# Performance work log

Hardware: AMD Instinct MI355X
Metric: run time of the kernel (lower is better)

Reference implementation:

```python
import jax, jax.numpy as jnp
import numpy as np

G = 64        # grid_size
S = 4         # num_samples along perpendicular axis
C = 771       # feature_channels
NH = 3        # n_heads
NV = 4        # number of camera views
HF = WF = 64  # image feature map size
B = 1
QD = 3 * C    # query_dim of TriplaneAttention


def bilin(img, gx, gy, padding):
    """Bilinear grid_sample, align_corners=True. img [C,H,W]; gx,gy normalized [-1,1]."""
    Ci, H, W = img.shape
    ix = (gx + 1.0) * 0.5 * (W - 1)
    iy = (gy + 1.0) * 0.5 * (H - 1)
    if padding == 'border':
        ix = jnp.clip(ix, 0, W - 1)
        iy = jnp.clip(iy, 0, H - 1)
    x0 = jnp.floor(ix); y0 = jnp.floor(iy)
    x1 = x0 + 1.0;      y1 = y0 + 1.0
    wx = ix - x0;       wy = iy - y0
    img2 = img.reshape(Ci, H * W)
    def gather(xi, yi):
        xc = jnp.clip(xi, 0, W - 1).astype(jnp.int32)
        yc = jnp.clip(yi, 0, H - 1).astype(jnp.int32)
        vals = jnp.take(img2, (yc * W + xc).reshape(-1), axis=1).reshape((Ci,) + xi.shape)
        if padding == 'zeros':
            valid = ((xi >= 0) & (xi <= W - 1) & (yi >= 0) & (yi <= H - 1)).astype(img.dtype)
            vals = vals * valid
        return vals
    return (gather(x0, y0) * ((1 - wx) * (1 - wy)) + gather(x1, y0) * (wx * (1 - wy))
            + gather(x0, y1) * ((1 - wx) * wy) + gather(x1, y1) * (wx * wy))


def sample_points_along_axis(plane):
    x = jnp.linspace(-1.0, 1.0, G)
    gx, gy = jnp.meshgrid(x, x, indexing='xy')  # [G,G]
    samp = jnp.linspace(-1.0, 1.0, S)
    ex = jnp.broadcast_to(gx[..., None], (G, G, S))
    ey = jnp.broadcast_to(gy[..., None], (G, G, S))
    es = jnp.broadcast_to(samp[None, None, :], (G, G, S))
    if plane == 'xy':
        return jnp.stack([ex, ey, es], axis=-1)
    elif plane == 'xz':
        return jnp.stack([ex, es, ey], axis=-1)
    else:
        return jnp.stack([es, ex, ey], axis=-1)


def project_to_other_planes(points, plane, queries):
    # points [G,G,S,3]; queries = [q_xy, q_xz, q_yz] each [G,G,C]
    idx = {'xy': 0, 'xz': 1, 'yz': 2}
    sel = {'xy': (0, 1), 'xz': (0, 2), 'yz': (1, 2)}
    feats = []
    for other in ['xy', 'xz', 'yz']:
        if other == plane:
            continue
        a, b = sel[other]
        coords = jnp.stack([points[..., a], points[..., b]], axis=-1)
        # Faithful to original: pixel-range coords passed as normalized grid, border padding
        g = jnp.clip((coords * 0.5 + 0.5) * (G - 1), 0, G - 1)
        pf = queries[idx[other]].transpose(2, 0, 1)  # [C,G,G]
        s = bilin(pf, g[..., 0], g[..., 1], 'border')  # [C,G,G,S]
        feats.append(s.transpose(1, 2, 3, 0))          # [G,G,S,C]
    return jnp.concatenate(feats, axis=2)              # [G,G,2S,C]


def layernorm(x, g, b):
    mu = jnp.mean(x, axis=-1, keepdims=True)
    var = jnp.mean((x - mu) ** 2, axis=-1, keepdims=True)
    return (x - mu) / jnp.sqrt(var + 1e-5) * g + b


def triplane_attention(query, context, Wk, bk, Wv, bv, ln_g, ln_b):
    # query [B,N,QD]; context [B,N,L,C]
    Bq, N, L, _ = context.shape
    DH = QD // NH
    q = layernorm(query, ln_g, ln_b).reshape(Bq, N, NH, DH)
    k = (context @ Wk + bk).reshape(Bq, N, L, NH, DH)
    v = (context @ Wv + bv).reshape(Bq, N, L, NH, DH)
    scores = jnp.einsum('bnlhd,bnhd->bhnl', k, q)   # no 1/sqrt(d) scaling (faithful)
    w = jax.nn.softmax(scores, axis=-1)
    out = jnp.einsum('bhnl,bnlhd->bnhd', w, v)
    return out.reshape(Bq, N, QD)


def setup_inputs():
    key = jax.random.key(0)
    ks = jax.random.split(key, 12)
    image_features = jax.random.normal(ks[0], (B, NV, C, HF, WF), jnp.float32)
    depths = jax.random.uniform(ks[1], (B, NV, HF, WF), jnp.float32)
    # cameras: identity rotation, w2c translation [dx,0,3] -> c2w translation [-dx,0,-3]
    offs = np.linspace(-0.2, 0.2, NV).astype(np.float32)
    c2w = np.tile(np.eye(4, dtype=np.float32), (B, NV, 1, 1))
    for m in range(NV):
        c2w[:, m, 0, 3] = -offs[m]
        c2w[:, m, 2, 3] = -3.0
    K = np.zeros((B, NV, 3, 3), np.float32)
    K[:, :, 0, 0] = WF; K[:, :, 1, 1] = HF
    K[:, :, 0, 2] = WF / 2; K[:, :, 1, 2] = HF / 2; K[:, :, 2, 2] = 1.0
    pointclouds = jax.random.uniform(ks[2], (B, 4096, 3), jnp.float32, minval=-1.0, maxval=1.0)
    q_xy = jax.random.normal(ks[3], (G, G, C), jnp.float32) * 0.02
    q_xz = jax.random.normal(ks[4], (G, G, C), jnp.float32) * 0.02
    q_yz = jax.random.normal(ks[5], (G, G, C), jnp.float32) * 0.02
    Wk = jax.random.normal(ks[6], (C, QD), jnp.float32) * 0.02
    bk = jnp.zeros((QD,), jnp.float32)
    Wv = jax.random.normal(ks[7], (C, QD), jnp.float32) * 0.02
    bv = jnp.zeros((QD,), jnp.float32)
    ln_g = jnp.ones((QD,), jnp.float32)
    ln_b = jnp.zeros((QD,), jnp.float32)
    return dict(image_features=image_features, depths=depths, c2w_cond=jnp.asarray(c2w),
                intrinsic_cond=jnp.asarray(K), pointclouds=pointclouds,
                q_xy=q_xy, q_xz=q_xz, q_yz=q_yz, Wk=Wk, bk=bk, Wv=Wv, bv=bv,
                ln_g=ln_g, ln_b=ln_b)


def _forward(image_features, c2w_cond, intrinsic_cond, q_xy, q_xz, q_yz,
             Wk, bk, Wv, bv, ln_g, ln_b):
    queries = [q_xy, q_xz, q_yz]
    w2c = jnp.linalg.inv(c2w_cond)  # [B,NV,4,4]

    def project(pts, w2c_b, K_b):
        # pts [N,3]; returns u,v,mask each [N,NV]
        ph = jnp.concatenate([pts, jnp.ones_like(pts[:, :1])], axis=-1)
        cam = jnp.einsum('nl,mkl->nmk', ph, w2c_b)      # [N,NV,4]
        depth = cam[..., 2]
        uvh = jnp.einsum('nmk,mhk->nmh', cam[..., :3], K_b)
        ds = depth + 1e-8
        u = uvh[..., 0] / ds
        v = uvh[..., 1] / ds
        mask = (depth > 0) & (u >= 0) & (u < WF) & (v >= 0) & (v < HF)
        return u, v, mask

    def sample_views(feats_b, u_b, v_b, mask_b):
        # feats_b [NV,C,HF,WF]; u_b,v_b [N,NV] -> [N,NV,C]
        gx = 2.0 * (u_b / (WF - 1)) - 1.0
        gy = 2.0 * (v_b / (HF - 1)) - 1.0
        samp = jax.vmap(lambda img, x, y: bilin(img, x, y, 'zeros'))(feats_b, gx.T, gy.T)  # [NV,C,N]
        samp = samp.transpose(2, 0, 1)  # [N,NV,C]
        return samp * mask_b[..., None].astype(samp.dtype)

    outs = []
    for pi, plane in enumerate(['xy', 'xz', 'yz']):
        points = sample_points_along_axis(plane)           # [G,G,S,3]
        pts = points.reshape(-1, 3)                        # [G*G*S,3]
        u, v, mask = jax.vmap(lambda w, k: project(pts, w, k))(w2c, intrinsic_cond)  # [B,N,NV]
        samp = jax.vmap(sample_views)(image_features, u, v, mask)  # [B,N,NV,C]
        ctx = samp.reshape(B, G * G, S * NV, C)
        other = project_to_other_planes(points, plane, queries)    # [G,G,2S,C]
        q = jnp.concatenate([queries[pi],
                             jnp.mean(other[:, :, :S], axis=2),
                             jnp.mean(other[:, :, S:], axis=2)], axis=-1).reshape(G * G, QD)
        q = jnp.broadcast_to(q[None], (B, G * G, QD))
        out = triplane_attention(q, ctx, Wk, bk, Wv, bv, ln_g, ln_b)
        outs.append(out.reshape(B, G, G, QD))
    return tuple(outs)


def reference(image_features, depths, c2w_cond, intrinsic_cond, pointclouds,
              q_xy, q_xz, q_yz, Wk, bk, Wv, bv, ln_g, ln_b):
    return _forward(image_features, c2w_cond, intrinsic_cond,
                    q_xy, q_xz, q_yz, Wk, bk, Wv, bv, ln_g, ln_b)
```

## Files before the change

kernel.cpp:

```cpp
#include <hip/hip_runtime.h>
#include <math.h>


constexpr int kG = 64, kS = 4, kC = 771, kNV = 4;
constexpr int kQD = 2313;
constexpr int kNPIX = 4096;
constexpr int kL = 16;
constexpr int kImgMStride = kC * kG * kG;
constexpr int kKP = 800;
constexpr int kLDA = 2400;
constexpr int kBROWS = 896;
constexpr int kCP = 776;
constexpr int kNG = kCP / 4;
constexpr int kLDQ = 3 * kCP;
constexpr int kIMS2 = kNPIX * kCP;

constexpr size_t kQKB_FLOATS = (size_t)kNPIX * kLDQ;
constexpr size_t kW_ELEMS = (size_t)3 * kBROWS * kKP;
constexpr size_t kA0_ELEMS = (size_t)kNPIX * kKP;
constexpr size_t kWH_ELEMS = (size_t)kNPIX * kLDA;
constexpr size_t kQN_FLOATS = (size_t)kNPIX * kQD;
constexpr size_t kTAB_FLOATS = (size_t)6 * 64 * kC;

using bf16x8 = __attribute__((ext_vector_type(8))) short;
using f32x4 = __attribute__((ext_vector_type(4))) float;

__device__ __forceinline__ unsigned short f2bf(float x) {
  unsigned int u = __float_as_uint(x);
  u = (u + 0x7FFFu + ((u >> 16) & 1u)) >> 16;
  return (unsigned short)u;
}
__device__ __forceinline__ float bf2f(unsigned short h) {
  return __uint_as_float(((unsigned int)h) << 16);
}
__device__ __forceinline__ void gload16(const unsigned short* g,
                                        unsigned short* l) {
  __builtin_amdgcn_global_load_lds(
      (const __attribute__((address_space(1))) void*)g,
      (__attribute__((address_space(3))) void*)l, 16, 0, 0);
}

__global__ void invert4_kernel(const float* __restrict__ c2w,
                               float* __restrict__ w2c) {
  const int m = threadIdx.x;
  if (m >= kNV) return;
  float a[4][8];
  for (int r = 0; r < 4; ++r)
    for (int c = 0; c < 4; ++c) {
      a[r][c] = c2w[m * 16 + r * 4 + c];
      a[r][4 + c] = (r == c) ? 1.f : 0.f;
    }
  for (int col = 0; col < 4; ++col) {
    int piv = col;
    float best = fabsf(a[col][col]);
    for (int r = col + 1; r < 4; ++r) {
      float t = fabsf(a[r][col]);
      if (t > best) { best = t; piv = r; }
    }
    if (piv != col)
      for (int c = 0; c < 8; ++c) {
        float t = a[col][c]; a[col][c] = a[piv][c]; a[piv][c] = t;
      }
    const float inv = 1.f / a[col][col];
    for (int c = 0; c < 8; ++c) a[col][c] *= inv;
    for (int r = 0; r < 4; ++r)
      if (r != col) {
        const float f = a[r][col];
        for (int c = 0; c < 8; ++c) a[r][c] -= f * a[col][c];
      }
  }
  for (int r = 0; r < 4; ++r)
    for (int c = 0; c < 4; ++c) w2c[m * 16 + r * 4 + c] = a[r][4 + c];
}

__global__ void __launch_bounds__(256) transpose_img_kernel(
    const float* __restrict__ img, float* __restrict__ out) {
  __shared__ float t[64][65];
  const int y = blockIdx.x, m = blockIdx.y, tid = threadIdx.x;
  const size_t obase = ((size_t)m * kNPIX + (size_t)y * 64) * kCP;
  for (int c0 = 0; c0 < kC; c0 += 64) {
    const int cw = (kC - c0) < 64 ? (kC - c0) : 64;
    for (int idx = tid; idx < cw * 64; idx += 256) {
      const int cl = idx >> 6, x = idx & 63;
      t[cl][x] = img[(((size_t)m * kC + c0 + cl) * 64 + y) * 64 + x];
    }
    __syncthreads();
    for (int idx = tid; idx < 64 * 64; idx += 256) {
      const int x = idx >> 6, cl = idx & 63;
      if (cl < cw) out[obase + (size_t)x * kCP + c0 + cl] = t[cl][x];
    }
    __syncthreads();
  }
  for (int idx = tid; idx < 64 * 8; idx += 256) {
    const int x = idx >> 3, c = 768 + (idx & 7);
    if (c >= kC && c < kCP) out[obase + (size_t)x * kCP + c] = 0.f;
  }
}

__global__ void __launch_bounds__(256) prep_wk_kernel(
    const float* __restrict__ Wk, unsigned short* __restrict__ hi,
// ... 23 lines not shown
    const int j = j0 + ty, k = k0 + tx;
    if (j < kBROWS && k < kKP) {
      const float v = t[tx][ty];
      const unsigned short a = f2bf(v);
      const size_t p = ((size_t)h * kBROWS + j) * kKP + k;
      hi[p] = a;
      lo[p] = f2bf(v - bf2f(a));
    }
  }
}

__global__ void __launch_bounds__(256) prep_meantab_kernel(
    const float* __restrict__ q_xy, const float* __restrict__ q_xz,
    const float* __restrict__ q_yz, float* __restrict__ tab) {
  const int v = blockIdx.x;
  const int t = blockIdx.y;
  const int plane = t >> 1, part = t & 1;
  const float* src;
  if (plane == 0) src = part ? q_yz : q_xz;
  else if (plane == 1) src = part ? q_yz : q_xy;
  else src = part ? q_xz : q_xy;
  __shared__ int sIdx[4][4];
  __shared__ float sW[4][4];
  if (threadIdx.x < 4) {
    const int s = threadIdx.x;
    const float Xv = -1.f + 2.f * v / 63.f;
    const float Ts = -1.f + 2.f * s / 3.f;
    float a, b;
    if (plane == 0) { a = Xv; b = Ts; }
    else if (plane == 1) {
      if (part == 0) { a = Xv; b = Ts; } else { a = Ts; b = Xv; }
    } else { a = Ts; b = Xv; }
    const float ga = fminf(fmaxf((a * 0.5f + 0.5f) * 63.f, 0.f), 63.f);
    const float gb = fminf(fmaxf((b * 0.5f + 0.5f) * 63.f, 0.f), 63.f);
    const float ix = fminf(fmaxf((ga + 1.f) * 0.5f * 63.f, 0.f), 63.f);
    const float iy = fminf(fmaxf((gb + 1.f) * 0.5f * 63.f, 0.f), 63.f);
    const float x0 = floorf(ix), y0 = floorf(iy);
    const float wx = ix - x0, wy = iy - y0;
    const int x0i = (int)x0, y0i = (int)y0;
    const int x1i = (x0i + 1 > 63) ? 63 : x0i + 1;
    const int y1i = (y0i + 1 > 63) ? 63 : y0i + 1;
    sIdx[s][0] = (y0i * 64 + x0i) * kC;
    sIdx[s][1] = (y0i * 64 + x1i) * kC;
    sIdx[s][2] = (y1i * 64 + x0i) * kC;
    sIdx[s][3] = (y1i * 64 + x1i) * kC;
    sW[s][0] = (1.f - wx) * (1.f - wy);
    sW[s][1] = wx * (1.f - wy);
    sW[s][2] = (1.f - wx) * wy;
    sW[s][3] = wx * wy;
  }
  __syncthreads();
  for (int c = threadIdx.x; c < kC; c += 256) {
    float a1 = 0.f;
#pragma unroll
    for (int s = 0; s < 4; ++s) {
      a1 += src[sIdx[s][0] + c] * sW[s][0] + src[sIdx[s][1] + c] * sW[s][1]
          + src[sIdx[s][2] + c] * sW[s][2] + src[sIdx[s][3] + c] * sW[s][3];
    }
    tab[((size_t)t * 64 + v) * kC + c] = a1 * 0.25f;
  }
}

__global__ void __launch_bounds__(256) prep_tabsplit_kernel(
    const float* __restrict__ tab, const float* __restrict__ ln_g,
    unsigned short* __restrict__ hi, unsigned short* __restrict__ lo) {
  const int v = blockIdx.x;
  const int t = blockIdx.y;
  const int h = 1 + (t & 1);
  const size_t base = ((size_t)t * 128 + v) * kKP;
  for (int k = threadIdx.x; k < kKP; k += 256) {
    float val = 0.f;
    if (v < 64 && k < kC)
      val = tab[((size_t)t * 64 + v) * kC + k] * ln_g[h * kC + k];
    const unsigned short a = f2bf(val);
    hi[base + k] = a;
    lo[base + k] = f2bf(val - bf2f(a));
  }
}

__global__ void __launch_bounds__(256) prep_uv_kernel(
    const float* __restrict__ Wk, const float* __restrict__ ln_g,
    const float* __restrict__ ln_b, float* __restrict__ u,
    float* __restrict__ v) {
  const int c = blockIdx.x * 256 + threadIdx.x;
  const int h = blockIdx.y;
  if (c >= kCP) return;
  float su = 0.f, sv = 0.f;
  if (c < kC) {
    const float* wr = Wk + (size_t)c * kQD + h * kC;
    const float* g = ln_g + h * kC;
    const float* b = ln_b + h * kC;
    for (int k = 0; k < kC; ++k) {
      su = fmaf(wr[k], g[k], su);
      sv = fmaf(wr[k], b[k], sv);
    }
  }
  u[h * kCP + c] = su;
  v[h * kCP + c] = sv;
}

__global__ void __launch_bounds__(256) build_a0_kernel(
    const float* __restrict__ q_xy, const float* __restrict__ q_xz,
    const float* __restrict__ q_yz, const float* __restrict__ tab,
    const float* __restrict__ ln_g, const float* __restrict__ ln_b,
    const float* __restrict__ bk, unsigned short* __restrict__ a0hi,
    unsigned short* __restrict__ a0lo, float* __restrict__ murs,
    float* __restrict__ qbk) {
  const int slot = blockIdx.y, plane = slot;
  const float* qp = (plane == 0) ? q_xy : (plane == 1) ? q_xz : q_yz;
  const int n = blockIdx.x, i = n >> 6, j = n & 63, tid = threadIdx.x;
  __shared__ float qf[kQD];
  __shared__ float red[16];

  const float* t0 = tab + ((size_t)(plane * 2 + 0) * 64 + j) * kC;
  const float* t1 = tab + ((size_t)(plane * 2 + 1) * 64 + i) * kC;
  for (int c = tid; c < kC; c += 256) {
    qf[c] = qp[(size_t)n * kC + c];
    qf[kC + c] = t0[c];
    qf[2 * kC + c] = t1[c];
  }
  __syncthreads();

  float sm = 0.f;
  for (int idx = tid; idx < kQD; idx += 256) sm += qf[idx];
#pragma unroll
  for (int off = 32; off; off >>= 1) sm += __shfl_down(sm, off);
  if ((tid & 63) == 0) red[tid >> 6] = sm;
  __syncthreads();
  const float mu = (red[0] + red[1] + red[2] + red[3]) * (1.f / kQD);
  __syncthreads();
  float sq = 0.f;
  for (int idx = tid; idx < kQD; idx += 256) {
    const float d = qf[idx] - mu;
    sq += d * d;
  }
#pragma unroll
  for (int off = 32; off; off >>= 1) sq += __shfl_down(sq, off);
  if ((tid & 63) == 0) red[tid >> 6] = sq;
  __syncthreads();
  const float var = (red[0] + red[1] + red[2] + red[3]) * (1.f / kQD);
  const float rstd = 1.f / sqrtf(var + 1e-5f);
  if (tid == 0) {
    murs[2 * ((size_t)slot * kNPIX + n)] = mu;
    murs[2 * ((size_t)slot * kNPIX + n) + 1] = rstd;
  }
  __syncthreads();

  float h0 = 0.f, h1 = 0.f, h2 = 0.f;
  unsigned short* ah = a0hi + (size_t)slot * kA0_ELEMS + (size_t)n * kKP;
  unsigned short* al = a0lo + (size_t)slot * kA0_ELEMS + (size_t)n * kKP;
  for (int idx = tid; idx < 3 * kKP; idx += 256) {
    int h, k;
    if (idx < kKP) { h = 0; k = idx; }
    else if (idx < 2 * kKP) { h = 1; k = idx - kKP; }
    else { h = 2; k = idx - 2 * kKP; }
    if (k < kC) {
      const int li = h * kC + k;
      const float v = (qf[li] - mu) * rstd * ln_g[li] + ln_b[li];
      const float pb = v * bk[li];
      if (h == 0) h0 += pb; else if (h == 1) h1 += pb; else h2 += pb;
    }
    if (idx < kKP) {
      const float y = (idx < kC) ? qf[idx] * ln_g[idx] : 0.f;
      const unsigned short hv = f2bf(y);
      ah[idx] = hv;
      al[idx] = f2bf(y - bf2f(hv));
    }
  }
#pragma unroll
  for (int off = 32; off; off >>= 1) {
    h0 += __shfl_down(h0, off);
    h1 += __shfl_down(h1, off);
    h2 += __shfl_down(h2, off);
  }
  if ((tid & 63) == 0) {
    red[(tid >> 6) * 4 + 0] = h0;
    red[(tid >> 6) * 4 + 1] = h1;
    red[(tid >> 6) * 4 + 2] = h2;
  }
  __syncthreads();
  if (tid < 3)
    qbk[((size_t)slot * kNPIX + n) * 3 + tid] =
        red[tid] + red[4 + tid] + red[8 + tid] + red[12 + tid];
}

__global__ void __launch_bounds__(256) gemm_a0_kernel(
    const unsigned short* __restrict__ A0hi,
    const unsigned short* __restrict__ A0lo,
    const unsigned short* __restrict__ Bhi,
    const unsigned short* __restrict__ Blo, const float* __restrict__ murs,
    const float* __restrict__ uvec, const float* __restrict__ vvec,
    float* __restrict__ qkb) {
  __shared__ unsigned short smA[2][128 * 32];
  __shared__ unsigned short smB[2][128 * 32];
  const int slot = blockIdx.z;
  const int t = blockIdx.y * 7 + blockIdx.x;
  const int xcd = t & 7, idx = t >> 3;
  const int nb = idx % 7, mb = (xcd << 2) + idx / 7;
  const int m0 = mb * 128, n0 = nb * 128;
  const unsigned short* Ah = A0hi + (size_t)slot * kA0_ELEMS;
  const unsigned short* Al = A0lo + (size_t)slot * kA0_ELEMS;
  const int tid = threadIdx.x;
  const int lane = tid & 63, w = tid >> 6;
  const int wm = w >> 1, wn = w & 1;

  const int sr0 = w * 16 + (lane >> 2);
  const int ss = lane & 3;
  size_t aoff[2], boff[2];
  int ldsb[2];
#pragma unroll
  for (int p = 0; p < 2; ++p) {
    const int r = p * 64 + sr0;
    const int kl = (ss ^ ((r >> 1) & 3)) * 8;
    aoff[p] = (size_t)(m0 + r) * kKP + kl;
    boff[p] = (size_t)(n0 + r) * kKP + kl;
    ldsb[p] = (p * 64 + w * 16) * 32;
  }
  int offA[4], offB[4];
#pragma unroll
  for (int i = 0; i < 4; ++i) {
    const int ra = wm * 64 + i * 16 + (lane & 15);
    offA[i] = ra * 32 + (((lane >> 4) ^ ((ra >> 1) & 3)) << 3);
    const int rb = wn * 64 + i * 16 + (lane & 15);
    offB[i] = rb * 32 + (((lane >> 4) ^ ((rb >> 1) & 3)) << 3);
  }
  f32x4 acc[4][4];
#pragma unroll
  for (int i = 0; i < 4; ++i)
#pragma unroll
    for (int j = 0; j < 4; ++j) acc[i][j] = f32x4{0.f, 0.f, 0.f, 0.f};

  for (int k0 = 0; k0 < kKP; k0 += 32) {
#pragma unroll
    for (int p = 0; p < 2; ++p) {
      gload16(Ah + aoff[p] + k0, &smA[0][ldsb[p]]);
      gload16(Al + aoff[p] + k0, &smA[1][ldsb[p]]);
      gload16(Bhi + boff[p] + k0, &smB[0][ldsb[p]]);
      gload16(Blo + boff[p] + k0, &smB[1][ldsb[p]]);
    }
    __syncthreads();
    bf16x8 ah[4], al[4], bh[4], bl[4];
#pragma unroll
    for (int i = 0; i < 4; ++i) {
      ah[i] = *(const bf16x8*)&smA[0][offA[i]];
      al[i] = *(const bf16x8*)&smA[1][offA[i]];
      bh[i] = *(const bf16x8*)&smB[0][offB[i]];
      bl[i] = *(const bf16x8*)&smB[1][offB[i]];
    }
#pragma unroll
    for (int i = 0; i < 4; ++i)
#pragma unroll
      for (int j = 0; j < 4; ++j)
        acc[i][j] = __builtin_amdgcn_mfma_f32_16x16x32_bf16(ah[i], bh[j],
                                                            acc[i][j], 0, 0, 0);
#pragma unroll
    for (int i = 0; i < 4; ++i)
#pragma unroll
      for (int j = 0; j < 4; ++j)
        acc[i][j] = __builtin_amdgcn_mfma_f32_16x16x32_bf16(ah[i], bl[j],
                                                            acc[i][j], 0, 0, 0);
#pragma unroll
    for (int i = 0; i < 4; ++i)
#pragma unroll
      for (int j = 0; j < 4; ++j)
        acc[i][j] = __builtin_amdgcn_mfma_f32_16x16x32_bf16(al[i], bh[j],
                                                            acc[i][j], 0, 0, 0);
    __syncthreads();
  }

  const float* mr = murs + 2 * ((size_t)slot * kNPIX);
  float* dst = qkb + (size_t)slot * kQKB_FLOATS;
  const int rbase = m0 + wm * 64;
  const int cbase = n0 + wn * 64;
#pragma unroll
  for (int i = 0; i < 4; ++i) {
#pragma unroll
    for (int j = 0; j < 4; ++j) {
      const int col = cbase + j * 16 + (lane & 15);
      if (col < kC) {
        const float uu = uvec[col], vv = vvec[col];
#pragma unroll
        for (int r = 0; r < 4; ++r) {
          const int row = rbase + i * 16 + (lane >> 4) * 4 + r;
          const float mu = mr[2 * row], rs = mr[2 * row + 1];
          dst[(size_t)row * kLDQ + col] =
              rs * acc[i][j][r] - rs * mu * uu + vv;
        }
      } else if (col < kCP) {
#pragma unroll
        for (int r = 0; r < 4; ++r) {
          const int row = rbase + i * 16 + (lane >> 4) * 4 + r;
          dst[(size_t)row * kLDQ + col] = 0.f;
        }
      }
    }
  }
}

__global__ void __launch_bounds__(256) gemm_tab_kernel(
    const unsigned short* __restrict__ Thi,
    const unsigned short* __restrict__ Tlo,
    const unsigned short* __restrict__ Wkhi,
    const unsigned short* __restrict__ Wklo, float* __restrict__ Atab) {
  __shared__ unsigned short smA[2][128 * 32];
  __shared__ unsigned short smB[2][128 * 32];
  const int t = blockIdx.y;
  const int n0 = blockIdx.x * 128;
  const int h = 1 + (t & 1);
  const unsigned short* Ah = Thi + (size_t)t * 128 * kKP;
  const unsigned short* Al = Tlo + (size_t)t * 128 * kKP;
  const unsigned short* Bh = Wkhi + (size_t)h * kBROWS * kKP;
  const unsigned short* Bl = Wklo + (size_t)h * kBROWS * kKP;
  const int tid = threadIdx.x;
  const int lane = tid & 63, w = tid >> 6;
  const int wm = w >> 1, wn = w & 1;

  const int sr0 = w * 16 + (lane >> 2);
  const int ss = lane & 3;
  size_t aoff[2], boff[2];
  int ldsb[2];
#pragma unroll
  for (int p = 0; p < 2; ++p) {
    const int r = p * 64 + sr0;
    const int kl = (ss ^ ((r >> 1) & 3)) * 8;
    aoff[p] = (size_t)r * kKP + kl;
    boff[p] = (size_t)(n0 + r) * kKP + kl;
    ldsb[p] = (p * 64 + w * 16) * 32;
  }
  int offA[4], offB[4];
#pragma unroll
  for (int i = 0; i < 4; ++i) {
    const int ra = wm * 64 + i * 16 + (lane & 15);
    offA[i] = ra * 32 + (((lane >> 4) ^ ((ra >> 1) & 3)) << 3);
    const int rb = wn * 64 + i * 16 + (lane & 15);
    offB[i] = rb * 32 + (((lane >> 4) ^ ((rb >> 1) & 3)) << 3);
  }
  f32x4 acc[4][4];
#pragma unroll
  for (int i = 0; i < 4; ++i)
#pragma unroll
    for (int j = 0; j < 4; ++j) acc[i][j] = f32x4{0.f, 0.f, 0.f, 0.f};

  for (int k0 = 0; k0 < kKP; k0 += 32) {
#pragma unroll
    for (int p = 0; p < 2; ++p) {
      gload16(Ah + aoff[p] + k0, &smA[0][ldsb[p]]);
      gload16(Al + aoff[p] + k0, &smA[1][ldsb[p]]);
      gload16(Bh + boff[p] + k0, &smB[0][ldsb[p]]);
      gload16(Bl + boff[p] + k0, &smB[1][ldsb[p]]);
    }
    __syncthreads();
    bf16x8 ah[4], al[4], bh[4], bl[4];
#pragma unroll
    for (int i = 0; i < 4; ++i) {
      ah[i] = *(const bf16x8*)&smA[0][offA[i]];
      al[i] = *(const bf16x8*)&smA[1][offA[i]];
      bh[i] = *(const bf16x8*)&smB[0][offB[i]];
      bl[i] = *(const bf16x8*)&smB[1][offB[i]];
    }
#pragma unroll
    for (int i = 0; i < 4; ++i)
#pragma unroll
      for (int j = 0; j < 4; ++j)
        acc[i][j] = __builtin_amdgcn_mfma_f32_16x16x32_bf16(ah[i], bh[j],
                                                            acc[i][j], 0, 0, 0);
#pragma unroll
    for (int i = 0; i < 4; ++i)
#pragma unroll
      for (int j = 0; j < 4; ++j)
        acc[i][j] = __builtin_amdgcn_mfma_f32_16x16x32_bf16(ah[i], bl[j],
                                                            acc[i][j], 0, 0, 0);
#pragma unroll
    for (int i = 0; i < 4; ++i)
#pragma unroll
      for (int j = 0; j < 4; ++j)
        acc[i][j] = __builtin_amdgcn_mfma_f32_16x16x32_bf16(al[i], bh[j],
                                                            acc[i][j], 0, 0, 0);
    __syncthreads();
  }

  float* C = Atab + (size_t)t * 128 * kCP;
  const int rbase = wm * 64;
  const int cbase = n0 + wn * 64;
#pragma unroll
  for (int i = 0; i < 4; ++i) {
#pragma unroll
    for (int j = 0; j < 4; ++j) {
      const int col = cbase + j * 16 + (lane & 15);
      if (col < kCP) {
        const float keep = (col < kC) ? 1.f : 0.f;
#pragma unroll
        for (int r = 0; r < 4; ++r) {
          const int row = rbase + i * 16 + (lane >> 4) * 4 + r;
          C[(size_t)row * kCP + col] = acc[i][j][r] * keep;
        }
      }
    }
  }
}

__global__ void __launch_bounds__(256) combine_qk_kernel(
    const float* __restrict__ Atab, const float* __restrict__ u,
    const float* __restrict__ v, const float* __restrict__ murs,
    float* __restrict__ qkb) {
  const int slot = blockIdx.y, n = blockIdx.x;
  const int i = n >> 6, j = n & 63, tid = threadIdx.x;
  const float mu = murs[2 * ((size_t)slot * kNPIX + n)];
  const float rs = murs[2 * ((size_t)slot * kNPIX + n) + 1];
  const float rsmu = rs * mu;
  float* dst = qkb + (size_t)slot * kQKB_FLOATS + (size_t)n * kLDQ;
  const float* A1 = Atab + ((size_t)(slot * 2 + 0) * 128 + j) * kCP;
  const float* A2 = Atab + ((size_t)(slot * 2 + 1) * 128 + i) * kCP;
  if (tid < kNG) {
    const int c4 = tid << 2;
    const float4 a1 = *(const float4*)&A1[c4];
    const float4 u1 = *(const float4*)&u[kCP + c4];
    const float4 v1 = *(const float4*)&v[kCP + c4];
    float4 r1;
    r1.x = rs * a1.x - rsmu * u1.x + v1.x;
    r1.y = rs * a1.y - rsmu * u1.y + v1.y;
    r1.z = rs * a1.z - rsmu * u1.z + v1.z;
    r1.w = rs * a1.w - rsmu * u1.w + v1.w;
    *(float4*)&dst[kCP + c4] = r1;
    const float4 a2 = *(const float4*)&A2[c4];
    const float4 u2 = *(const float4*)&u[2 * kCP + c4];
    const float4 v2 = *(const float4*)&v[2 * kCP + c4];
    float4 r2;
    r2.x = rs * a2.x - rsmu * u2.x + v2.x;
    r2.y = rs * a2.y - rsmu * u2.y + v2.y;
    r2.z = rs * a2.z - rsmu * u2.z + v2.z;
    r2.w = rs * a2.w - rsmu * u2.w + v2.w;
    *(float4*)&dst[2 * kCP + c4] = r2;
  }
}

__global__ void __launch_bounds__(512, 6) sample_attn4_kernel(
    const float* __restrict__ imgt, const float* __restrict__ w2c,
    const float* __restrict__ Kin, const float* __restrict__ qkb,
    const float* __restrict__ qbk, const int plane_base,
    unsigned short* __restrict__ whi) {
  __shared__ __align__(16) float ctx[kL][kCP];
  __shared__ float sW2[kL][4];
  __shared__ int sI2[kL][4];
  __shared__ float sscp[2][48];
  __shared__ float ssc[48], swt[48];
  const int slot = blockIdx.y, plane = plane_base + slot;
  const int bid = blockIdx.x;
  const int n = ((bid & 7) << 9) | (bid >> 3);
  const int i = n >> 6, j = n & 63, tid = threadIdx.x;
  const float* qkn = qkb + (size_t)slot * kQKB_FLOATS + (size_t)n * kLDQ;

  if (tid < kL) {
    const int s = tid >> 2, m = tid & 3;
    const float Xi = -1.f + 2.f * i / 63.f;
    const float Xj = -1.f + 2.f * j / 63.f;
    const float Ts = -1.f + 2.f * s / 3.f;
    float px, py, pz;
    if (plane == 0) { px = Xj; py = Xi; pz = Ts; }
    else if (plane == 1) { px = Xj; py = Ts; pz = Xi; }
    else { px = Ts; py = Xj; pz = Xi; }
    const float* W = w2c + m * 16;
    const float c0 = W[0] * px + W[1] * py + W[2] * pz + W[3];
    const float c1 = W[4] * px + W[5] * py + W[6] * pz + W[7];
    const float c2 = W[8] * px + W[9] * py + W[10] * pz + W[11];
    const float* Km = Kin + m * 9;
    const float un = Km[0] * c0 + Km[1] * c1 + Km[2] * c2;
    const float vn = Km[3] * c0 + Km[4] * c1 + Km[5] * c2;
    const float ds = c2 + 1e-8f;
    const float u = un / ds, v = vn / ds;
    const bool mk =
        (c2 > 0.f && u >= 0.f && u < 64.f && v >= 0.f && v < 64.f);
    float w00 = 0.f, w10 = 0.f, w01 = 0.f, w11 = 0.f;
    int i00 = 0, i10 = 0, i01 = 0, i11 = 0;
    if (mk) {
      const float gx = 2.f * (u / 63.f) - 1.f;
      const float gy = 2.f * (v / 63.f) - 1.f;
      const float ix = (gx + 1.f) * 0.5f * 63.f;
      const float iy = (gy + 1.f) * 0.5f * 63.f;
      const float x0 = floorf(ix), y0 = floorf(iy);
      const float x1 = x0 + 1.f, y1 = y0 + 1.f;
      const float wx = ix - x0, wy = iy - y0;
      const float v00 = (x0 >= 0.f && x0 <= 63.f && y0 >= 0.f && y0 <= 63.f) ? 1.f : 0.f;
      const float v10 = (x1 >= 0.f && x1 <= 63.f && y0 >= 0.f && y0 <= 63.f) ? 1.f : 0.f;
      const float v01 = (x0 >= 0.f && x0 <= 63.f && y1 >= 0.f && y1 <= 63.f) ? 1.f : 0.f;
      const float v11 = (x1 >= 0.f && x1 <= 63.f && y1 >= 0.f && y1 <= 63.f) ? 1.f : 0.f;
      w00 = (1.f - wx) * (1.f - wy) * v00;
      w10 = wx * (1.f - wy) * v10;
      w01 = (1.f - wx) * wy * v01;
      w11 = wx * wy * v11;
      const int x0i = (int)fminf(fmaxf(x0, 0.f), 63.f);
      const int x1i = (int)fminf(fmaxf(x1, 0.f), 63.f);
      const int y0i = (int)fminf(fmaxf(y0, 0.f), 63.f);
      const int y1i = (int)fminf(fmaxf(y1, 0.f), 63.f);
      const int mb = m * kIMS2;
      i00 = mb + (y0i * 64 + x0i) * kCP;
      i10 = mb + (y0i * 64 + x1i) * kCP;
      i01 = mb + (y1i * 64 + x0i) * kCP;
      i11 = mb + (y1i * 64 + x1i) * kCP;
    }
    sI2[tid][0] = i00; sI2[tid][1] = i10; sI2[tid][2] = i01; sI2[tid][3] = i11;
    sW2[tid][0] = w00; sW2[tid][1] = w10; sW2[tid][2] = w01; sW2[tid][3] = w11;
  }
  __syncthreads();

  const int lane = tid & 63, wv = tid >> 6;
#pragma unroll
  for (int q = 0; q < 2; ++q) {
    const int l = (wv << 1) + q;
    const float a0 = sW2[l][0], a1 = sW2[l][1], a2 = sW2[l][2], a3 = sW2[l][3];
    const int b0 = sI2[l][0], b1 = sI2[l][1], b2 = sI2[l][2], b3 = sI2[l][3];
    for (int g = lane; g < kNG; g += 64) {
      const int c4 = g << 2;
      const float4 t0 = *(const float4*)&imgt[b0 + c4];
      const float4 t1 = *(const float4*)&imgt[b1 + c4];
      const float4 t2 = *(const float4*)&imgt[b2 + c4];
      const float4 t3 = *(const float4*)&imgt[b3 + c4];
      float4 r;
      r.x = fmaf(t0.x, a0, fmaf(t1.x, a1, fmaf(t2.x, a2, t3.x * a3)));
      r.y = fmaf(t0.y, a0, fmaf(t1.y, a1, fmaf(t2.y, a2, t3.y * a3)));
      r.z = fmaf(t0.z, a0, fmaf(t1.z, a1, fmaf(t2.z, a2, t3.z * a3)));
      r.w = fmaf(t0.w, a0, fmaf(t1.w, a1, fmaf(t2.w, a2, t3.w * a3)));
      *(float4*)&ctx[l][c4] = r;
    }
  }
  __syncthreads();

  const int g16 = tid >> 4, l16 = tid & 15;
  const float* qbkn = qbk + ((size_t)slot * kNPIX + n) * 3;
  {
    const int l = g16 & 15, half = g16 >> 4;
    float p0 = 0.f, p1 = 0.f, p2 = 0.f;
#pragma unroll
    for (int it = 0; it < 6; ++it) {
      const int c4 = (l16 + ((2 * it + half) << 4)) << 2;
      const float4 cv = *(const float4*)&ctx[l][c4];
      const float4 q0 = *(const float4*)&qkn[c4];
      const float4 q1 = *(const float4*)&qkn[kCP + c4];
      const float4 q2 = *(const float4*)&qkn[2 * kCP + c4];
      p0 = fmaf(cv.x, q0.x, fmaf(cv.y, q0.y, fmaf(cv.z, q0.z, fmaf(cv.w, q0.w, p0))));
      p1 = fmaf(cv.x, q1.x, fmaf(cv.y, q1.y, fmaf(cv.z, q1.z, fmaf(cv.w, q1.w, p1))));
      p2 = fmaf(cv.x, q2.x, fmaf(cv.y, q2.y, fmaf(cv.z, q2.z, fmaf(cv.w, q2.w, p2))));
    }
    if (half == 0 && l16 < 2) {
      const int c4 = (192 + l16) << 2;
      const float4 cv = *(const float4*)&ctx[l][c4];
      const float4 q0 = *(const float4*)&qkn[c4];
      const float4 q1 = *(const float4*)&qkn[kCP + c4];
      const float4 q2 = *(const float4*)&qkn[2 * kCP + c4];
      p0 = fmaf(cv.x, q0.x, fmaf(cv.y, q0.y, fmaf(cv.z, q0.z, fmaf(cv.w, q0.w, p0))));
      p1 = fmaf(cv.x, q1.x, fmaf(cv.y, q1.y, fmaf(cv.z, q1.z, fmaf(cv.w, q1.w, p1))));
      p2 = fmaf(cv.x, q2.x, fmaf(cv.y, q2.y, fmaf(cv.z, q2.z, fmaf(cv.w, q2.w, p2))));
    }
#pragma unroll
    for (int off = 8; off; off >>= 1) {
      p0 += __shfl_down(p0, off, 16);
      p1 += __shfl_down(p1, off, 16);
      p2 += __shfl_down(p2, off, 16);
    }
    if (l16 == 0) {
      sscp[half][l] = p0;
      sscp[half][16 + l] = p1;
      sscp[half][32 + l] = p2;
    }
  }
  __syncthreads();
  if (tid < 48) ssc[tid] = sscp[0][tid] + sscp[1][tid] + qbkn[tid >> 4];
  __syncthreads();
  if (tid < 3) {
    float mx = ssc[tid * 16];
#pragma unroll
    for (int l = 1; l < kL; ++l) mx = fmaxf(mx, ssc[tid * 16 + l]);
    float e[kL];
    float sum = 0.f;
#pragma unroll
    for (int l = 0; l < kL; ++l) {
      e[l] = expf(ssc[tid * 16 + l] - mx);
      sum += e[l];
    }
    const float inv = 1.f / sum;
#pragma unroll
    for (int l = 0; l < kL; ++l) swt[tid * 16 + l] = e[l] * inv;
  }
  __syncthreads();

  unsigned short* wh = whi + (size_t)slot * kWH_ELEMS + (size_t)n * kLDA;
  if (tid < 2 * kNG) {
    const int c4 = (tid >> 1) << 2;
    const int l0 = (tid & 1) << 3;
    float4 o0{0.f, 0.f, 0.f, 0.f}, o1{0.f, 0.f, 0.f, 0.f},
        o2{0.f, 0.f, 0.f, 0.f};
#pragma unroll
    for (int dl = 0; dl < 8; ++dl) {
      const int l = l0 + dl;
      const float4 cv = *(const float4*)&ctx[l][c4];
      const float s0 = swt[l], s1 = swt[16 + l], s2 = swt[32 + l];
      o0.x = fmaf(cv.x, s0, o0.x); o0.y = fmaf(cv.y, s0, o0.y);
      o0.z = fmaf(cv.z, s0, o0.z); o0.w = fmaf(cv.w, s0, o0.w);
      o1.x = fmaf(cv.x, s1, o1.x); o1.y = fmaf(cv.y, s1, o1.y);
      o1.z = fmaf(cv.z, s1, o1.z); o1.w = fmaf(cv.w, s1, o1.w);
      o2.x = fmaf(cv.x, s2, o2.x); o2.y = fmaf(cv.y, s2, o2.y);
      o2.z = fmaf(cv.z, s2, o2.z); o2.w = fmaf(cv.w, s2, o2.w);
    }
    o0.x += __shfl_xor(o0.x, 1); o0.y += __shfl_xor(o0.y, 1);
    o0.z += __shfl_xor(o0.z, 1); o0.w += __shfl_xor(o0.w, 1);
    o1.x += __shfl_xor(o1.x, 1); o1.y += __shfl_xor(o1.y, 1);
    o1.z += __shfl_xor(o1.z, 1); o1.w += __shfl_xor(o1.w, 1);
    o2.x += __shfl_xor(o2.x, 1); o2.y += __shfl_xor(o2.y, 1);
    o2.z += __shfl_xor(o2.z, 1); o2.w += __shfl_xor(o2.w, 1);
    if ((tid & 1) == 0) {
      float4 ov[3] = {o0, o1, o2};
#pragma unroll
      for (int h = 0; h < 3; ++h) {
        ushort4 hi;
        hi.x = f2bf(ov[h].x);
        hi.y = f2bf(ov[h].y);
        hi.z = f2bf(ov[h].z);
        hi.w = f2bf(ov[h].w);
        *(ushort4*)&wh[h * kKP + c4] = hi;
      }
    }
  }
  if (tid < 72) {
    const int h = tid / 24, k2 = kCP + tid % 24;
    wh[h * kKP + k2] = 0;
  }
}

__global__ void __launch_bounds__(256) gemm_out_kernel(
    const unsigned short* __restrict__ Ahi,
    const unsigned short* __restrict__ Bhi,
    const unsigned short* __restrict__ Blo, float* __restrict__ C,
    const float* __restrict__ bias) {
  __shared__ unsigned short smA[128 * 32];
  __shared__ unsigned short smB[2][128 * 32];
  const int slot = blockIdx.z / 3, h = blockIdx.z % 3;
  const int t = blockIdx.y * 7 + blockIdx.x;
  const int xcd = t & 7, idx = t >> 3;
  const int nb = idx % 7, mb = (xcd << 2) + idx / 7;
  const int m0 = mb * 128, n0 = nb * 128;
  const unsigned short* Ah = Ahi + (size_t)slot * kWH_ELEMS;
  float* Cs = C + (size_t)slot * kQN_FLOATS;
  const int tid = threadIdx.x;
  const int lane = tid & 63, w = tid >> 6;
  const int wm = w >> 1, wn = w & 1;

// ... 341 lines not shown
      float v = 0.f;
      if (k0 + kk < K) v = A[(size_t)(m0 + mm) * lda + hoff + k0 + kk];
      As[kk][mm] = v;
    }
    if (BT) {
#pragma unroll
      for (int p = 0; p < 4; ++p) {
        const int idx = tid + p * 256;
        const int jj = idx >> 4, kk = idx & 15;
        float v = 0.f;
        if ((n0 + jj) < N && (k0 + kk) < K)
          v = B[(size_t)(n0 + jj) * ldb + hoff + k0 + kk];
        Bs[kk][jj] = v;
      }
    } else {
#pragma unroll
      for (int p = 0; p < 4; ++p) {
        const int idx = tid + p * 256;
        const int kk = idx >> 6, jj = idx & 63;
        float v = 0.f;
        if ((n0 + jj) < N && (k0 + kk) < K)
          v = B[(size_t)(k0 + kk) * ldb + hoff + n0 + jj];
        Bs[kk][jj] = v;
      }
    }
    __syncthreads();
#pragma unroll
    for (int kk = 0; kk < BK; ++kk) {
      float a[8], b[4];
#pragma unroll
      for (int r = 0; r < 8; ++r) a[r] = As[kk][ty * 8 + r];
#pragma unroll
      for (int c = 0; c < 4; ++c) b[c] = Bs[kk][tx * 4 + c];
#pragma unroll
      for (int r = 0; r < 8; ++r)
#pragma unroll
        for (int c = 0; c < 4; ++c) acc[r][c] = fmaf(a[r], b[c], acc[r][c]);
    }
    __syncthreads();
  }
#pragma unroll
  for (int r = 0; r < 8; ++r) {
    const int mm = m0 + ty * 8 + r;
    if (mm >= M) continue;
#pragma unroll
    for (int c = 0; c < 4; ++c) {
      const int jj = n0 + tx * 4 + c;
      if (jj < N) {
        float v = acc[r][c];
        if (BIAS) v += bias[hoff + jj];
        Cp[(size_t)mm * ldc + hoff + jj] = v;
      }
    }
  }
}

extern "C" void kernel_launch(void* const* d_in, const int* in_sizes, int n_in,
                              void* d_out, int out_size, void* d_ws,
                              size_t ws_size, hipStream_t stream) {
  const float* imgf = (const float*)d_in[0];
  const float* c2w = (const float*)d_in[2];
  const float* Kin = (const float*)d_in[3];
  const float* qpl[3] = {(const float*)d_in[5], (const float*)d_in[6],
                         (const float*)d_in[7]};
  const float* Wk = (const float*)d_in[8];
  const float* bk = (const float*)d_in[9];
  const float* Wv = (const float*)d_in[10];
  const float* bv = (const float*)d_in[11];
  const float* ln_g = (const float*)d_in[12];
  const float* ln_b = (const float*)d_in[13];
  float* out = (float*)d_out;
  char* wsb = (char*)d_ws;

  const size_t IMGT_FLOATS = (size_t)kNV * kIMS2;

  size_t off = 0;
  auto take = [&](size_t bytes) {
    size_t p = off;
    off = (off + bytes + 511) & ~(size_t)511;
    return p;
  };
  const size_t o_w2c = take(64 * 4);
  const size_t o_qbk = take((size_t)3 * kNPIX * 3 * 4);
  const size_t o_qkb = take((size_t)3 * kQKB_FLOATS * 4);
  const size_t o_wkhi = take(kW_ELEMS * 2);
  const size_t o_wklo = take(kW_ELEMS * 2);
  const size_t o_wvthi = take(kW_ELEMS * 2);
  const size_t o_wvtlo = take(kW_ELEMS * 2);
  const size_t o_a0hi = take((size_t)3 * kA0_ELEMS * 2);
  const size_t o_a0lo = take((size_t)3 * kA0_ELEMS * 2);
  const size_t o_whi = take((size_t)3 * kWH_ELEMS * 2);
  const size_t o_murs = take((size_t)3 * kNPIX * 2 * 4);
  const size_t o_u = take((size_t)3 * kCP * 4);
  const size_t o_v = take((size_t)3 * kCP * 4);
  const size_t o_tab = take(kTAB_FLOATS * 4);
  const size_t o_tshi = take((size_t)6 * 128 * kKP * 2);
  const size_t o_tslo = take((size_t)6 * 128 * kKP * 2);
  const size_t o_atab = take((size_t)6 * 128 * kCP * 4);
  const size_t o_imgt = take(IMGT_FLOATS * 4);
  const size_t need = off;

  if (ws_size >= need) {
    float* w2c = (float*)(wsb + o_w2c);
    float* qbk = (float*)(wsb + o_qbk);
    float* qkb = (float*)(wsb + o_qkb);
    unsigned short* wkhi = (unsigned short*)(wsb + o_wkhi);
    unsigned short* wklo = (unsigned short*)(wsb + o_wklo);
    unsigned short* wvthi = (unsigned short*)(wsb + o_wvthi);
    unsigned short* wvtlo = (unsigned short*)(wsb + o_wvtlo);
    unsigned short* a0hi = (unsigned short*)(wsb + o_a0hi);
    unsigned short* a0lo = (unsigned short*)(wsb + o_a0lo);
    unsigned short* whi = (unsigned short*)(wsb + o_whi);
    float* murs = (float*)(wsb + o_murs);
    float* uvec = (float*)(wsb + o_u);
    float* vvec = (float*)(wsb + o_v);
    float* meantab = (float*)(wsb + o_tab);
    unsigned short* tshi = (unsigned short*)(wsb + o_tshi);
    unsigned short* tslo = (unsigned short*)(wsb + o_tslo);
    float* atab = (float*)(wsb + o_atab);
    float* imgt = (float*)(wsb + o_imgt);

    invert4_kernel<<<1, 64, 0, stream>>>(c2w, w2c);
    prep_wk_kernel<<<dim3(kBROWS, 3), 256, 0, stream>>>(Wk, wkhi, wklo);
    prep_wvt_kernel<<<dim3(13, 14, 3), 256, 0, stream>>>(Wv, wvthi, wvtlo);
    prep_meantab_kernel<<<dim3(64, 6), 256, 0, stream>>>(qpl[0], qpl[1],
                                                         qpl[2], meantab);
    prep_tabsplit_kernel<<<dim3(128, 6), 256, 0, stream>>>(meantab, ln_g,
                                                           tshi, tslo);
    prep_uv_kernel<<<dim3(4, 3), 256, 0, stream>>>(Wk, ln_g, ln_b, uvec,
                                                   vvec);
    transpose_img_kernel<<<dim3(64, kNV), 256, 0, stream>>>(imgf, imgt);
    gemm_tab_kernel<<<dim3(7, 6), 256, 0, stream>>>(tshi, tslo, wkhi, wklo,
                                                    atab);
    build_a0_kernel<<<dim3(kNPIX, 3), 256, 0, stream>>>(
        qpl[0], qpl[1], qpl[2], meantab, ln_g, ln_b, bk, a0hi, a0lo, murs,
        qbk);
    gemm_a0_kernel<<<dim3(7, 32, 3), 256, 0, stream>>>(
        a0hi, a0lo, wkhi, wklo, murs, uvec, vvec, qkb);
    combine_qk_kernel<<<dim3(kNPIX, 3), 256, 0, stream>>>(atab, uvec, vvec,
                                                          murs, qkb);
    sample_attn4_kernel<<<dim3(kNPIX, 3), 512, 0, stream>>>(
        imgt, w2c, Kin, qkb, qbk, 0, whi);
    gemm_out_kernel<<<dim3(7, 32, 9), 256, 0, stream>>>(whi, wvthi, wvtlo,
                                                        out, bv);
  } else {
    float* ws = (float*)d_ws;
    const size_t OFF_QBK = 64;
    const size_t OFF_BIG = OFF_QBK + (size_t)kNPIX * 3;
    float* w2c = ws;
    float* qbk = ws + OFF_QBK;
    float* qn = ws + OFF_BIG;
    float* qkb = qn + kQN_FLOATS;

    invert4_kernel<<<1, 64, 0, stream>>>(c2w, w2c);
    for (int p = 0; p < 3; ++p) {
      build_q_f32<<<kNPIX, 256, 0, stream>>>(qpl[0], qpl[1], qpl[2], p, ln_g,
                                             ln_b, bk, qn, qbk);
      gemm_f32<true, false><<<dim3(13, 32, 3), 256, 0, stream>>>(
          qn, Wk, qkb, nullptr, kNPIX, kC, kC, kQD, kQD, kQD, kC);
      sample_attn_f32<<<kNPIX, 256, 0, stream>>>(imgf, w2c, Kin, qkb, qbk, p,
                                                 qn);
      gemm_f32<false, true><<<dim3(13, 32, 3), 256, 0, stream>>>(
          qn, Wv, out + (size_t)p * kQN_FLOATS, bv, kNPIX, kC, kC, kQD, kQD,
          kQD, kC);
    }
  }
}
```

Measured before the change: 710.9 us.

## Fuse q/k combine into attention kernel and parallelize u/v prep reduction

Removes the combine_qk kernel that wrote full per-pixel q·Wk for the two mean-derived heads. The attention kernel now reads the small shared table rows, u and v directly and applies the per-pixel scale algebraically after the dot products. This cuts a large intermediate buffer write and read in exchange for more dot products per context row. It also rewrites prep_uv so each block reduces one output column across threads instead of having one thread loop serially over all 771 inputs.

```diff
diff --git a/kernel.cpp b/kernel.cpp
--- a/kernel.cpp
+++ b/kernel.cpp
@@ -12,10 +12,9 @@
 constexpr int kBROWS = 896;
 constexpr int kCP = 776;
 constexpr int kNG = kCP / 4;
-constexpr int kLDQ = 3 * kCP;
 constexpr int kIMS2 = kNPIX * kCP;
 
-constexpr size_t kQKB_FLOATS = (size_t)kNPIX * kLDQ;
+constexpr size_t kQ0_FLOATS = (size_t)kNPIX * kCP;
 constexpr size_t kW_ELEMS = (size_t)3 * kBROWS * kKP;
 constexpr size_t kA0_ELEMS = (size_t)kNPIX * kKP;
 constexpr size_t kWH_ELEMS = (size_t)kNPIX * kLDA;
@@ -205,21 +204,34 @@
     const float* __restrict__ Wk, const float* __restrict__ ln_g,
     const float* __restrict__ ln_b, float* __restrict__ u,
     float* __restrict__ v) {
-  const int c = blockIdx.x * 256 + threadIdx.x;
+  const int c = blockIdx.x;
   const int h = blockIdx.y;
-  if (c >= kCP) return;
+  __shared__ float ru[4], rv[4];
   float su = 0.f, sv = 0.f;
   if (c < kC) {
     const float* wr = Wk + (size_t)c * kQD + h * kC;
     const float* g = ln_g + h * kC;
     const float* b = ln_b + h * kC;
-    for (int k = 0; k < kC; ++k) {
-      su = fmaf(wr[k], g[k], su);
-      sv = fmaf(wr[k], b[k], sv);
-    }
-  }
-  u[h * kCP + c] = su;
-  v[h * kCP + c] = sv;
+    for (int k = threadIdx.x; k < kC; k += 256) {
+      const float w = wr[k];
+      su = fmaf(w, g[k], su);
+      sv = fmaf(w, b[k], sv);
+    }
+  }
+#pragma unroll
+  for (int off = 32; off; off >>= 1) {
+    su += __shfl_down(su, off);
+    sv += __shfl_down(sv, off);
+  }
+  if ((threadIdx.x & 63) == 0) {
+    ru[threadIdx.x >> 6] = su;
+    rv[threadIdx.x >> 6] = sv;
+  }
+  __syncthreads();
+  if (threadIdx.x == 0) {
+    u[h * kCP + c] = ru[0] + ru[1] + ru[2] + ru[3];
+    v[h * kCP + c] = rv[0] + rv[1] + rv[2] + rv[3];
+  }
 }
 
 __global__ void __launch_bounds__(256) build_a0_kernel(
@@ -313,7 +325,7 @@
     const unsigned short* __restrict__ Bhi,
     const unsigned short* __restrict__ Blo, const float* __restrict__ murs,
     const float* __restrict__ uvec, const float* __restrict__ vvec,
-    float* __restrict__ qkb) {
+    float* __restrict__ qk0) {
   __shared__ unsigned short smA[2][128 * 32];
   __shared__ unsigned short smB[2][128 * 32];
   const int slot = blockIdx.z;
@@ -392,7 +404,7 @@
   }
 
   const float* mr = murs + 2 * ((size_t)slot * kNPIX);
-  float* dst = qkb + (size_t)slot * kQKB_FLOATS;
+  float* dst = qk0 + (size_t)slot * kQ0_FLOATS;
   const int rbase = m0 + wm * 64;
   const int cbase = n0 + wn * 64;
 #pragma unroll
@@ -406,14 +418,13 @@
         for (int r = 0; r < 4; ++r) {
           const int row = rbase + i * 16 + (lane >> 4) * 4 + r;
           const float mu = mr[2 * row], rs = mr[2 * row + 1];
-          dst[(size_t)row * kLDQ + col] =
-              rs * acc[i][j][r] - rs * mu * uu + vv;
+          dst[(size_t)row * kCP + col] = rs * acc[i][j][r] - rs * mu * uu + vv;
         }
       } else if (col < kCP) {
 #pragma unroll
         for (int r = 0; r < 4; ++r) {
           const int row = rbase + i * 16 + (lane >> 4) * 4 + r;
-          dst[(size_t)row * kLDQ + col] = 0.f;
+          dst[(size_t)row * kCP + col] = 0.f;
         }
       }
     }
@@ -522,56 +533,21 @@
   }
 }
 
-__global__ void __launch_bounds__(256) combine_qk_kernel(
-    const float* __restrict__ Atab, const float* __restrict__ u,
-    const float* __restrict__ v, const float* __restrict__ murs,
-    float* __restrict__ qkb) {
-  const int slot = blockIdx.y, n = blockIdx.x;
-  const int i = n >> 6, j = n & 63, tid = threadIdx.x;
-  const float mu = murs[2 * ((size_t)slot * kNPIX + n)];
-  const float rs = murs[2 * ((size_t)slot * kNPIX + n) + 1];
-  const float rsmu = rs * mu;
-  float* dst = qkb + (size_t)slot * kQKB_FLOATS + (size_t)n * kLDQ;
-  const float* A1 = Atab + ((size_t)(slot * 2 + 0) * 128 + j) * kCP;
-  const float* A2 = Atab + ((size_t)(slot * 2 + 1) * 128 + i) * kCP;
-  if (tid < kNG) {
-    const int c4 = tid << 2;
-    const float4 a1 = *(const float4*)&A1[c4];
-    const float4 u1 = *(const float4*)&u[kCP + c4];
-    const float4 v1 = *(const float4*)&v[kCP + c4];
-    float4 r1;
-    r1.x = rs * a1.x - rsmu * u1.x + v1.x;
-    r1.y = rs * a1.y - rsmu * u1.y + v1.y;
-    r1.z = rs * a1.z - rsmu * u1.z + v1.z;
-    r1.w = rs * a1.w - rsmu * u1.w + v1.w;
-    *(float4*)&dst[kCP + c4] = r1;
-    const float4 a2 = *(const float4*)&A2[c4];
-    const float4 u2 = *(const float4*)&u[2 * kCP + c4];
-    const float4 v2 = *(const float4*)&v[2 * kCP + c4];
-    float4 r2;
-    r2.x = rs * a2.x - rsmu * u2.x + v2.x;
-    r2.y = rs * a2.y - rsmu * u2.y + v2.y;
-    r2.z = rs * a2.z - rsmu * u2.z + v2.z;
-    r2.w = rs * a2.w - rsmu * u2.w + v2.w;
-    *(float4*)&dst[2 * kCP + c4] = r2;
-  }
-}
-
-__global__ void __launch_bounds__(512, 6) sample_attn4_kernel(
+__global__ void __launch_bounds__(512, 6) sample_attn5_kernel(
     const float* __restrict__ imgt, const float* __restrict__ w2c,
-    const float* __restrict__ Kin, const float* __restrict__ qkb,
-    const float* __restrict__ qbk, const int plane_base,
-    unsigned short* __restrict__ whi) {
+    const float* __restrict__ Kin, const float* __restrict__ qk0,
+    const float* __restrict__ atab, const float* __restrict__ uvec,
+    const float* __restrict__ vvec, const float* __restrict__ murs,
+    const float* __restrict__ qbk, unsigned short* __restrict__ whi) {
   __shared__ __align__(16) float ctx[kL][kCP];
   __shared__ float sW2[kL][4];
   __shared__ int sI2[kL][4];
   __shared__ float sscp[2][48];
   __shared__ float ssc[48], swt[48];
-  const int slot = blockIdx.y, plane = plane_base + slot;
+  const int slot = blockIdx.y, plane = slot;
   const int bid = blockIdx.x;
   const int n = ((bid & 7) << 9) | (bid >> 3);
   const int i = n >> 6, j = n & 63, tid = threadIdx.x;
-  const float* qkn = qkb + (size_t)slot * kQKB_FLOATS + (size_t)n * kLDQ;
 
   if (tid < kL) {
     const int s = tid >> 2, m = tid & 3;
@@ -650,40 +626,54 @@
 
   const int g16 = tid >> 4, l16 = tid & 15;
   const float* qbkn = qbk + ((size_t)slot * kNPIX + n) * 3;
+  const float* qk0n = qk0 + (size_t)slot * kQ0_FLOATS + (size_t)n * kCP;
+  const float* A1r = atab + ((size_t)(slot * 2 + 0) * 128 + j) * kCP;
+  const float* A2r = atab + ((size_t)(slot * 2 + 1) * 128 + i) * kCP;
+  const float* u1 = uvec + kCP;
+  const float* u2 = uvec + 2 * kCP;
+  const float* v1 = vvec + kCP;
+  const float* v2 = vvec + 2 * kCP;
+  const float mun = murs[2 * ((size_t)slot * kNPIX + n)];
+  const float rsn = murs[2 * ((size_t)slot * kNPIX + n) + 1];
+  const float rsmu = rsn * mun;
   {
     const int l = g16 & 15, half = g16 >> 4;
-    float p0 = 0.f, p1 = 0.f, p2 = 0.f;
-#pragma unroll
-    for (int it = 0; it < 6; ++it) {
-      const int c4 = (l16 + ((2 * it + half) << 4)) << 2;
+    float p0 = 0.f, pa1 = 0.f, pu1 = 0.f, pv1 = 0.f;
+    float pa2 = 0.f, pu2 = 0.f, pv2 = 0.f;
+    auto dot7 = [&](int c4) {
       const float4 cv = *(const float4*)&ctx[l][c4];
-      const float4 q0 = *(const float4*)&qkn[c4];
-      const float4 q1 = *(const float4*)&qkn[kCP + c4];
-      const float4 q2 = *(const float4*)&qkn[2 * kCP + c4];
+      const float4 q0 = *(const float4*)&qk0n[c4];
+      const float4 xa1 = *(const float4*)&A1r[c4];
+      const float4 xu1 = *(const float4*)&u1[c4];
+      const float4 xv1 = *(const float4*)&v1[c4];
+      const float4 xa2 = *(const float4*)&A2r[c4];
+      const float4 xu2 = *(const float4*)&u2[c4];
+      const float4 xv2 = *(const float4*)&v2[c4];
       p0 = fmaf(cv.x, q0.x, fmaf(cv.y, q0.y, fmaf(cv.z, q0.z, fmaf(cv.w, q0.w, p0))));
-      p1 = fmaf(cv.x, q1.x, fmaf(cv.y, q1.y, fmaf(cv.z, q1.z, fmaf(cv.w, q1.w, p1))));
-      p2 = fmaf(cv.x, q2.x, fmaf(cv.y, q2.y, fmaf(cv.z, q2.z, fmaf(cv.w, q2.w, p2))));
-    }
-    if (half == 0 && l16 < 2) {
-      const int c4 = (192 + l16) << 2;
-      const float4 cv = *(const float4*)&ctx[l][c4];
-      const float4 q0 = *(const float4*)&qkn[c4];
-      const float4 q1 = *(const float4*)&qkn[kCP + c4];
-      const float4 q2 = *(const float4*)&qkn[2 * kCP + c4];
-      p0 = fmaf(cv.x, q0.x, fmaf(cv.y, q0.y, fmaf(cv.z, q0.z, fmaf(cv.w, q0.w, p0))));
-      p1 = fmaf(cv.x, q1.x, fmaf(cv.y, q1.y, fmaf(cv.z, q1.z, fmaf(cv.w, q1.w, p1))));
-      p2 = fmaf(cv.x, q2.x, fmaf(cv.y, q2.y, fmaf(cv.z, q2.z, fmaf(cv.w, q2.w, p2))));
-    }
+      pa1 = fmaf(cv.x, xa1.x, fmaf(cv.y, xa1.y, fmaf(cv.z, xa1.z, fmaf(cv.w, xa1.w, pa1))));
+      pu1 = fmaf(cv.x, xu1.x, fmaf(cv.y, xu1.y, fmaf(cv.z, xu1.z, fmaf(cv.w, xu1.w, pu1))));
+      pv1 = fmaf(cv.x, xv1.x, fmaf(cv.y, xv1.y, fmaf(cv.z, xv1.z, fmaf(cv.w, xv1.w, pv1))));
+      pa2 = fmaf(cv.x, xa2.x, fmaf(cv.y, xa2.y, fmaf(cv.z, xa2.z, fmaf(cv.w, xa2.w, pa2))));
+      pu2 = fmaf(cv.x, xu2.x, fmaf(cv.y, xu2.y, fmaf(cv.z, xu2.z, fmaf(cv.w, xu2.w, pu2))));
+      pv2 = fmaf(cv.x, xv2.x, fmaf(cv.y, xv2.y, fmaf(cv.z, xv2.z, fmaf(cv.w, xv2.w, pv2))));
+    };
+#pragma unroll
+    for (int it = 0; it < 6; ++it) dot7((l16 + ((2 * it + half) << 4)) << 2);
+    if (half == 0 && l16 < 2) dot7((192 + l16) << 2);
 #pragma unroll
     for (int off = 8; off; off >>= 1) {
       p0 += __shfl_down(p0, off, 16);
-      p1 += __shfl_down(p1, off, 16);
-      p2 += __shfl_down(p2, off, 16);
+      pa1 += __shfl_down(pa1, off, 16);
+      pu1 += __shfl_down(pu1, off, 16);
+      pv1 += __shfl_down(pv1, off, 16);
+      pa2 += __shfl_down(pa2, off, 16);
+      pu2 += __shfl_down(pu2, off, 16);
+      pv2 += __shfl_down(pv2, off, 16);
     }
     if (l16 == 0) {
       sscp[half][l] = p0;
-      sscp[half][16 + l] = p1;
-      sscp[half][32 + l] = p2;
+      sscp[half][16 + l] = rsn * pa1 - rsmu * pu1 + pv1;
+      sscp[half][32 + l] = rsn * pa2 - rsmu * pu2 + pv2;
     }
   }
   __syncthreads();
@@ -1191,7 +1181,7 @@
   };
   const size_t o_w2c = take(64 * 4);
   const size_t o_qbk = take((size_t)3 * kNPIX * 3 * 4);
-  const size_t o_qkb = take((size_t)3 * kQKB_FLOATS * 4);
+  const size_t o_qk0 = take((size_t)3 * kQ0_FLOATS * 4);
   const size_t o_wkhi = take(kW_ELEMS * 2);
   const size_t o_wklo = take(kW_ELEMS * 2);
   const size_t o_wvthi = take(kW_ELEMS * 2);
@@ -1212,7 +1202,7 @@
   if (ws_size >= need) {
     float* w2c = (float*)(wsb + o_w2c);
     float* qbk = (float*)(wsb + o_qbk);
-    float* qkb = (float*)(wsb + o_qkb);
+    float* qk0 = (float*)(wsb + o_qk0);
     unsigned short* wkhi = (unsigned short*)(wsb + o_wkhi);
     unsigned short* wklo = (unsigned short*)(wsb + o_wklo);
     unsigned short* wvthi = (unsigned short*)(wsb + o_wvthi);
@@ -1236,8 +1226,8 @@
                                                          qpl[2], meantab);
     prep_tabsplit_kernel<<<dim3(128, 6), 256, 0, stream>>>(meantab, ln_g,
                                                            tshi, tslo);
-    prep_uv_kernel<<<dim3(4, 3), 256, 0, stream>>>(Wk, ln_g, ln_b, uvec,
-                                                   vvec);
+    prep_uv_kernel<<<dim3(kCP, 3), 256, 0, stream>>>(Wk, ln_g, ln_b, uvec,
+                                                     vvec);
     transpose_img_kernel<<<dim3(64, kNV), 256, 0, stream>>>(imgf, imgt);
     gemm_tab_kernel<<<dim3(7, 6), 256, 0, stream>>>(tshi, tslo, wkhi, wklo,
                                                     atab);
@@ -1245,11 +1235,9 @@
         qpl[0], qpl[1], qpl[2], meantab, ln_g, ln_b, bk, a0hi, a0lo, murs,
         qbk);
     gemm_a0_kernel<<<dim3(7, 32, 3), 256, 0, stream>>>(
-        a0hi, a0lo, wkhi, wklo, murs, uvec, vvec, qkb);
-    combine_qk_kernel<<<dim3(kNPIX, 3), 256, 0, stream>>>(atab, uvec, vvec,
-                                                          murs, qkb);
-    sample_attn4_kernel<<<dim3(kNPIX, 3), 512, 0, stream>>>(
-        imgt, w2c, Kin, qkb, qbk, 0, whi);
+        a0hi, a0lo, wkhi, wklo, murs, uvec, vvec, qk0);
+    sample_attn5_kernel<<<dim3(kNPIX, 3), 512, 0, stream>>>(
+        imgt, w2c, Kin, qk0, atab, uvec, vvec, murs, qbk, whi);
     gemm_out_kernel<<<dim3(7, 32, 9), 256, 0, stream>>>(whi, wvthi, wvtlo,
                                                         out, bv);
   } else {
```

Measured after the change: 669.9 us. 5.8% less time.
